# Performance work log

Hardware: AMD Instinct MI355X
Metric: run time of the kernel (lower is better)

Reference implementation:

```python
import jax, jax.numpy as jnp
import numpy as np

SIZE = 1024      # codebook size
DIM = 64         # latent_dim
TOPK = 3
BETA_C = 0.25
LEGACY = False

def setup_inputs() -> dict:
    key = jax.random.key(0)
    kz, ke = jax.random.split(key)
    z = jax.random.normal(kz, (16, 64, 64, DIM), dtype=jnp.float32)
    # nn.Embedding init: uniform(-1/size, 1/size)
    emb = jax.random.uniform(ke, (SIZE, DIM), minval=-1.0 / SIZE, maxval=1.0 / SIZE, dtype=jnp.float32)
    return {"z": z, "emb": emb}

def reference(z, emb):
    zf = z.reshape(-1, DIM)                                  # [N, D]
    # squared euclidean distances via matmul expansion: [N, SIZE]
    d = (jnp.sum(zf ** 2, axis=1, keepdims=True)
         + jnp.sum(emb ** 2, axis=1)
         - 2.0 * (zf @ emb.T))
    neg_d, topk_idx = jax.lax.top_k(-d, TOPK)                # smallest distances -> [N, K]
    # direct gather instead of one-hot matmul (same math)
    z_q = jnp.mean(emb[topk_idx], axis=1).reshape(z.shape)   # [N,K,D] -> [N,D] -> z.shape
    if LEGACY:
        loss = (jnp.mean((jax.lax.stop_gradient(z_q) - z) ** 2)
                + BETA_C * jnp.mean((z_q - jax.lax.stop_gradient(z)) ** 2))
    else:
        loss = (BETA_C * jnp.mean((jax.lax.stop_gradient(z_q) - z) ** 2)
                + jnp.mean((z_q - jax.lax.stop_gradient(z)) ** 2))
    # one-hot encodings are part of the module's return signature
    topk_encodings = jax.nn.one_hot(topk_idx, SIZE, dtype=z.dtype)   # [N, K, SIZE]
    e_mean = jnp.mean(topk_encodings, axis=(0, 1))                   # [SIZE]
    perplexity = jnp.exp(-jnp.sum(e_mean * jnp.log(e_mean + 1e-10)))
    z_q_st = z + jax.lax.stop_gradient(z_q - z)              # straight-through estimator
    return (z_q_st, loss, perplexity, topk_encodings, topk_idx)
```

## Files before the change

### kernel.cpp

```cpp
#include <hip/hip_runtime.h>
#include <math.h>

#define N_ROWS 65536
#define CB 1024
#define SPLITS 4
#define JS (CB / SPLITS)

__device__ __forceinline__ float tree_sum64_sq(const float* x) {
#pragma clang fp contract(off)
    float sq[64];
#pragma unroll
    for (int i = 0; i < 64; ++i) sq[i] = x[i] * x[i];
    float s[16];
#pragma unroll
    for (int l = 0; l < 16; ++l) s[l] = (sq[l] + sq[l + 16]) + (sq[l + 32] + sq[l + 48]);
    float t[8];
#pragma unroll
    for (int l = 0; l < 8; ++l) t[l] = s[l] + s[l + 8];
    float u[4];
#pragma unroll
    for (int l = 0; l < 4; ++l) u[l] = t[l] + t[l + 4];
    float v0 = u[0] + u[2];
    float v1 = u[1] + u[3];
    return v0 + v1;
}

__device__ __forceinline__ void top3_insert(float d, int j,
                                            float& v0, float& v1, float& v2,
                                            int& i0, int& i1, int& i2) {
    bool b0 = d < v0, b1 = d < v1, b2 = d < v2;
    v2 = b1 ? v1 : (b2 ? d : v2);
    i2 = b1 ? i1 : (b2 ? j : i2);
    v1 = b0 ? v0 : (b1 ? d : v1);
    i1 = b0 ? i0 : (b1 ? j : i1);
    v0 = b0 ? d : v0;
    i0 = b0 ? j : i0;
}

__global__ __launch_bounds__(256) void embB_kernel(const float* __restrict__ emb,
                                                   float* __restrict__ B) {
    int j = blockIdx.x * 256 + threadIdx.x;
    if (j >= CB) return;
    float e[64];
    const float4* e4 = (const float4*)(emb + (size_t)j * 64);
#pragma unroll
    for (int k = 0; k < 16; ++k) {
        float4 v = e4[k];
        e[4 * k] = v.x; e[4 * k + 1] = v.y; e[4 * k + 2] = v.z; e[4 * k + 3] = v.w;
    }
    B[j] = tree_sum64_sq(e);
}

__global__ __launch_bounds__(256) void score_kernel(const float* __restrict__ z,
                                                    const float* __restrict__ emb,
                                                    const float* __restrict__ B,
                                                    float* __restrict__ scrD,
                                                    int* __restrict__ scrI) {
    int bid = blockIdx.x;
    int split = bid & (SPLITS - 1);
    int rowBlk = bid >> 2;
    int row = rowBlk * 256 + threadIdx.x;

    float zr[64];
    const float4* z4 = (const float4*)(z + (size_t)row * 64);
#pragma unroll
    for (int k = 0; k < 16; ++k) {
        float4 v = z4[k];
        zr[4 * k] = v.x; zr[4 * k + 1] = v.y; zr[4 * k + 2] = v.z; zr[4 * k + 3] = v.w;
    }
    float A = tree_sum64_sq(zr);

    float v0 = 3.402823466e38f, v1 = 3.402823466e38f, v2 = 3.402823466e38f;
    int i0 = 0, i1 = 0, i2 = 0;
    int jbase = split * JS;

    for (int jj = 0; jj < JS; ++jj) {
        int j = jbase + jj;
        const float4* e4 = (const float4*)(emb + (size_t)j * 64);
        float Bj = B[j];
        float acc = 0.0f;
#pragma unroll
        for (int k = 0; k < 16; ++k) {
            float4 e = e4[k];
            acc = fmaf(zr[4 * k],     e.x, acc);
            acc = fmaf(zr[4 * k + 1], e.y, acc);
            acc = fmaf(zr[4 * k + 2], e.z, acc);
            acc = fmaf(zr[4 * k + 3], e.w, acc);
        }
        float d = (A + Bj) - 2.0f * acc;
        top3_insert(d, j, v0, v1, v2, i0, i1, i2);
    }
    size_t o = ((size_t)split * N_ROWS + row) * 3;
    scrD[o] = v0; scrD[o + 1] = v1; scrD[o + 2] = v2;
    scrI[o] = i0; scrI[o + 1] = i1; scrI[o + 2] = i2;
}

__global__ __launch_bounds__(256) void merge_kernel(const float* __restrict__ z,
                                                    const float* __restrict__ emb,
                                                    const float* __restrict__ scrD,
                                                    const int* __restrict__ scrI,
                                                    float* __restrict__ out0,
                                                    float* __restrict__ out4,
                                                    int* __restrict__ hist,
                                                    float* __restrict__ lossAcc) {
    int row = blockIdx.x * 256 + threadIdx.x;

    float v0 = 3.402823466e38f, v1 = 3.402823466e38f, v2 = 3.402823466e38f;
    int i0 = 0, i1 = 0, i2 = 0;
#pragma unroll
    for (int s = 0; s < SPLITS; ++s) {
        size_t o = ((size_t)s * N_ROWS + row) * 3;
#pragma unroll
        for (int t = 0; t < 3; ++t) {
            float d = scrD[o + t];
            int j = scrI[o + t];
            top3_insert(d, j, v0, v1, v2, i0, i1, i2);
        }
    }

    const float* e0 = emb + (size_t)i0 * 64;
    const float* e1 = emb + (size_t)i1 * 64;
    const float* e2 = emb + (size_t)i2 * 64;
    const float4* z4 = (const float4*)(z + (size_t)row * 64);
    float4* o4 = (float4*)(out0 + (size_t)row * 64);

    float lsum = 0.0f;
#pragma unroll
    for (int k4 = 0; k4 < 16; ++k4) {
        float4 zv = z4[k4];
        float4 st;
        {
            int k = 4 * k4;
            float zq = ((e0[k] + e1[k]) + e2[k]) / 3.0f;
            float df = zq - zv.x;
            st.x = zv.x + df;
            lsum = fmaf(df, df, lsum);
        }
        {
            int k = 4 * k4 + 1;
            float zq = ((e0[k] + e1[k]) + e2[k]) / 3.0f;
            float df = zq - zv.y;
            st.y = zv.y + df;
            lsum = fmaf(df, df, lsum);
        }
        {
            int k = 4 * k4 + 2;
            float zq = ((e0[k] + e1[k]) + e2[k]) / 3.0f;
            float df = zq - zv.z;
            st.z = zv.z + df;
            lsum = fmaf(df, df, lsum);
        }
        {
            int k = 4 * k4 + 3;
            float zq = ((e0[k] + e1[k]) + e2[k]) / 3.0f;
            float df = zq - zv.w;
            st.w = zv.w + df;
            lsum = fmaf(df, df, lsum);
        }
        o4[k4] = st;
    }

    size_t ob = (size_t)row * 3;
    out4[ob]     = (float)i0;
    out4[ob + 1] = (float)i1;
    out4[ob + 2] = (float)i2;
    atomicAdd(&hist[i0], 1);
    atomicAdd(&hist[i1], 1);
    atomicAdd(&hist[i2], 1);

#pragma unroll
    for (int off = 32; off >= 1; off >>= 1) lsum += __shfl_down(lsum, off);
    if ((threadIdx.x & 63) == 0) atomicAdd(lossAcc, lsum);
}

__global__ __launch_bounds__(256) void onehot_kernel(const float* __restrict__ idxf,
                                                     float4* __restrict__ out3) {
    size_t q = (size_t)blockIdx.x * 256 + threadIdx.x;
    int slice = (int)(q >> 8);
    int c0 = (int)(q & 255) * 4;
    int idx = (int)idxf[slice];
    float4 v;
    v.x = (c0     == idx) ? 1.0f : 0.0f;
    v.y = (c0 + 1 == idx) ? 1.0f : 0.0f;
    v.z = (c0 + 2 == idx) ? 1.0f : 0.0f;
    v.w = (c0 + 3 == idx) ? 1.0f : 0.0f;
    out3[q] = v;
}

__global__ __launch_bounds__(256) void finalize_kernel(const int* __restrict__ hist,
                                                       const float* __restrict__ lossAcc,
                                                       float* __restrict__ out1,
                                                       float* __restrict__ out2) {
    __shared__ float red[256];
    int t = threadIdx.x;
    float local = 0.0f;
    for (int b = t; b < CB; b += 256) {
        float em = (float)hist[b] / 196608.0f;
        local += em * logf(em + 1e-10f);
    }
    red[t] = local;
    __syncthreads();
    for (int s = 128; s >= 1; s >>= 1) {
        if (t < s) red[t] += red[t + s];
        __syncthreads();
    }
    if (t == 0) {
        *out2 = expf(-red[0]);
        float m = *lossAcc / 4194304.0f;
        *out1 = 0.25f * m + m;
    }
}

extern "C" void kernel_launch(void* const* d_in, const int* in_sizes, int n_in,
                              void* d_out, int out_size, void* d_ws, size_t ws_size,
                              hipStream_t stream) {
    const float* z   = (const float*)d_in[0];
    const float* emb = (const float*)d_in[1];

    float* out  = (float*)d_out;
    float* out0 = out;
    float* out1 = out + 4194304;
    float* out2 = out + 4194305;
    float* out3 = out + 4194306;
    float* out4 = out + 4194306 + 201326592ll;

    int*   hist    = (int*)d_ws;
    float* lossAcc = (float*)((char*)d_ws + 4096);
    float* B       = (float*)((char*)d_ws + 8192);

    float* scrD = out3;
    int*   scrI = (int*)(out3 + (size_t)SPLITS * N_ROWS * 3);

    hipMemsetAsync(d_ws, 0, 4096 + 16, stream);

    embB_kernel<<<4, 256, 0, stream>>>(emb, B);
    score_kernel<<<(N_ROWS / 256) * SPLITS, 256, 0, stream>>>(z, emb, B, scrD, scrI);
    merge_kernel<<<N_ROWS / 256, 256, 0, stream>>>(z, emb, scrD, scrI, out0, out4,
                                                   hist, lossAcc);
    onehot_kernel<<<196608, 256, 0, stream>>>(out4, (float4*)out3);
    finalize_kernel<<<1, 256, 0, stream>>>(hist, lossAcc, out1, out2);
}
```

Baseline: 1.076 ms.

## Fuse score and merge kernels via shared memory, align one-hot stores

Merges the split scoring and the top-3 merge into one kernel. Each block handles 64 rows with 4 codebook splits held in threads, and the partial top-3 results are combined in shared memory rather than through a global scratch buffer. The memset is folded into the prep kernel. The one-hot writer becomes a grid-stride loop with 16-byte-aligned nontemporal stores, offset by 2 floats because out3 is misaligned, with the edge elements fixed up separately. The combine step leaves 3/4 of each block's threads idle, and scoring now runs with 64 rows per block.

```diff
diff --git a/kernel.cpp b/kernel.cpp
--- a/kernel.cpp
+++ b/kernel.cpp
@@ -5,6 +5,8 @@
 #define CB 1024
 #define SPLITS 4
 #define JS (CB / SPLITS)
+
+typedef float v4f __attribute__((ext_vector_type(4)));
 
 __device__ __forceinline__ float tree_sum64_sq(const float* x) {
 #pragma clang fp contract(off)
@@ -37,8 +39,10 @@
     i0 = b0 ? j : i0;
 }
 
-__global__ __launch_bounds__(256) void embB_kernel(const float* __restrict__ emb,
-                                                   float* __restrict__ B) {
+__global__ __launch_bounds__(256) void prep_kernel(const float* __restrict__ emb,
+                                                   float* __restrict__ B,
+                                                   int* __restrict__ hist,
+                                                   float* __restrict__ lossAcc) {
     int j = blockIdx.x * 256 + threadIdx.x;
     if (j >= CB) return;
     float e[64];
@@ -49,17 +53,24 @@
         e[4 * k] = v.x; e[4 * k + 1] = v.y; e[4 * k + 2] = v.z; e[4 * k + 3] = v.w;
     }
     B[j] = tree_sum64_sq(e);
-}
-
-__global__ __launch_bounds__(256) void score_kernel(const float* __restrict__ z,
+    hist[j] = 0;
+    if (j == 0) *lossAcc = 0.0f;
+}
+
+__global__ __launch_bounds__(256) void fused_kernel(const float* __restrict__ z,
                                                     const float* __restrict__ emb,
                                                     const float* __restrict__ B,
-                                                    float* __restrict__ scrD,
-                                                    int* __restrict__ scrI) {
-    int bid = blockIdx.x;
-    int split = bid & (SPLITS - 1);
-    int rowBlk = bid >> 2;
-    int row = rowBlk * 256 + threadIdx.x;
+                                                    float* __restrict__ out0,
+                                                    float* __restrict__ out4,
+                                                    int* __restrict__ hist,
+                                                    float* __restrict__ lossAcc) {
+    __shared__ float sD[SPLITS][64][3];
+    __shared__ int   sI[SPLITS][64][3];
+
+    int t = threadIdx.x;
+    int r = t & 63;
+    int split = t >> 6;
+    int row = blockIdx.x * 64 + r;
 
     float zr[64];
     const float4* z4 = (const float4*)(z + (size_t)row * 64);
@@ -90,101 +101,85 @@
         float d = (A + Bj) - 2.0f * acc;
         top3_insert(d, j, v0, v1, v2, i0, i1, i2);
     }
-    size_t o = ((size_t)split * N_ROWS + row) * 3;
-    scrD[o] = v0; scrD[o + 1] = v1; scrD[o + 2] = v2;
-    scrI[o] = i0; scrI[o + 1] = i1; scrI[o + 2] = i2;
-}
-
-__global__ __launch_bounds__(256) void merge_kernel(const float* __restrict__ z,
-                                                    const float* __restrict__ emb,
-                                                    const float* __restrict__ scrD,
-                                                    const int* __restrict__ scrI,
-                                                    float* __restrict__ out0,
-                                                    float* __restrict__ out4,
-                                                    int* __restrict__ hist,
-                                                    float* __restrict__ lossAcc) {
-    int row = blockIdx.x * 256 + threadIdx.x;
-
-    float v0 = 3.402823466e38f, v1 = 3.402823466e38f, v2 = 3.402823466e38f;
-    int i0 = 0, i1 = 0, i2 = 0;
-#pragma unroll
-    for (int s = 0; s < SPLITS; ++s) {
-        size_t o = ((size_t)s * N_ROWS + row) * 3;
-#pragma unroll
-        for (int t = 0; t < 3; ++t) {
-            float d = scrD[o + t];
-            int j = scrI[o + t];
-            top3_insert(d, j, v0, v1, v2, i0, i1, i2);
+
+    sD[split][r][0] = v0; sD[split][r][1] = v1; sD[split][r][2] = v2;
+    sI[split][r][0] = i0; sI[split][r][1] = i1; sI[split][r][2] = i2;
+    __syncthreads();
+
+    if (t < 64) {
+        float m0 = 3.402823466e38f, m1 = 3.402823466e38f, m2 = 3.402823466e38f;
+        int j0 = 0, j1 = 0, j2 = 0;
+#pragma unroll
+        for (int s = 0; s < SPLITS; ++s) {
+#pragma unroll
+            for (int u = 0; u < 3; ++u)
+                top3_insert(sD[s][r][u], sI[s][r][u], m0, m1, m2, j0, j1, j2);
         }
-    }
-
-    const float* e0 = emb + (size_t)i0 * 64;
-    const float* e1 = emb + (size_t)i1 * 64;
-    const float* e2 = emb + (size_t)i2 * 64;
-    const float4* z4 = (const float4*)(z + (size_t)row * 64);
-    float4* o4 = (float4*)(out0 + (size_t)row * 64);
-
-    float lsum = 0.0f;
-#pragma unroll
-    for (int k4 = 0; k4 < 16; ++k4) {
-        float4 zv = z4[k4];
-        float4 st;
-        {
-            int k = 4 * k4;
-            float zq = ((e0[k] + e1[k]) + e2[k]) / 3.0f;
-            float df = zq - zv.x;
-            st.x = zv.x + df;
-            lsum = fmaf(df, df, lsum);
+
+        const float4* e0q = (const float4*)(emb + (size_t)j0 * 64);
+        const float4* e1q = (const float4*)(emb + (size_t)j1 * 64);
+        const float4* e2q = (const float4*)(emb + (size_t)j2 * 64);
+        v4f* o4 = (v4f*)(out0 + (size_t)row * 64);
+
+        float lsum = 0.0f;
+#pragma unroll
+        for (int k4 = 0; k4 < 16; ++k4) {
+            float4 a = e0q[k4], b = e1q[k4], c = e2q[k4];
+            float zx = zr[4 * k4], zy = zr[4 * k4 + 1];
+            float zz = zr[4 * k4 + 2], zw = zr[4 * k4 + 3];
+            v4f st;
+            float zq, df;
+            zq = ((a.x + b.x) + c.x) / 3.0f; df = zq - zx; st.x = zx + df; lsum = fmaf(df, df, lsum);
+            zq = ((a.y + b.y) + c.y) / 3.0f; df = zq - zy; st.y = zy + df; lsum = fmaf(df, df, lsum);
+            zq = ((a.z + b.z) + c.z) / 3.0f; df = zq - zz; st.z = zz + df; lsum = fmaf(df, df, lsum);
+            zq = ((a.w + b.w) + c.w) / 3.0f; df = zq - zw; st.w = zw + df; lsum = fmaf(df, df, lsum);
+            __builtin_nontemporal_store(st, o4 + k4);
         }
-        {
-            int k = 4 * k4 + 1;
-            float zq = ((e0[k] + e1[k]) + e2[k]) / 3.0f;
-            float df = zq - zv.y;
-            st.y = zv.y + df;
-            lsum = fmaf(df, df, lsum);
-        }
-        {
-            int k = 4 * k4 + 2;
-            float zq = ((e0[k] + e1[k]) + e2[k]) / 3.0f;
-            float df = zq - zv.z;
-            st.z = zv.z + df;
-            lsum = fmaf(df, df, lsum);
-        }
-        {
-            int k = 4 * k4 + 3;
-            float zq = ((e0[k] + e1[k]) + e2[k]) / 3.0f;
-            float df = zq - zv.w;
-            st.w = zv.w + df;
-            lsum = fmaf(df, df, lsum);
-        }
-        o4[k4] = st;
-    }
-
-    size_t ob = (size_t)row * 3;
-    out4[ob]     = (float)i0;
-    out4[ob + 1] = (float)i1;
-    out4[ob + 2] = (float)i2;
-    atomicAdd(&hist[i0], 1);
-    atomicAdd(&hist[i1], 1);
-    atomicAdd(&hist[i2], 1);
-
-#pragma unroll
-    for (int off = 32; off >= 1; off >>= 1) lsum += __shfl_down(lsum, off);
-    if ((threadIdx.x & 63) == 0) atomicAdd(lossAcc, lsum);
-}
-
+
+        size_t ob = (size_t)row * 3;
+        out4[ob]     = (float)j0;
+        out4[ob + 1] = (float)j1;
+        out4[ob + 2] = (float)j2;
+        atomicAdd(&hist[j0], 1);
+        atomicAdd(&hist[j1], 1);
+        atomicAdd(&hist[j2], 1);
+
+#pragma unroll
+        for (int off = 32; off >= 1; off >>= 1) lsum += __shfl_down(lsum, off);
+        if ((t & 63) == 0) atomicAdd(lossAcc, lsum);
+    }
+}
+
+#define OH_GRID 2048
 __global__ __launch_bounds__(256) void onehot_kernel(const float* __restrict__ idxf,
-                                                     float4* __restrict__ out3) {
-    size_t q = (size_t)blockIdx.x * 256 + threadIdx.x;
-    int slice = (int)(q >> 8);
-    int c0 = (int)(q & 255) * 4;
-    int idx = (int)idxf[slice];
-    float4 v;
-    v.x = (c0     == idx) ? 1.0f : 0.0f;
-    v.y = (c0 + 1 == idx) ? 1.0f : 0.0f;
-    v.z = (c0 + 2 == idx) ? 1.0f : 0.0f;
-    v.w = (c0 + 3 == idx) ? 1.0f : 0.0f;
-    out3[q] = v;
+                                                     float* __restrict__ out3f) {
+    v4f* o4 = (v4f*)(out3f + 2);
+    const int M = (N_ROWS * 3 * CB - 2) / 4;
+    const int stride = OH_GRID * 256;
+
+    for (int m = blockIdx.x * 256 + threadIdx.x; m < M; m += stride) {
+        int e0 = 2 + 4 * m;
+        int s0 = e0 >> 10;
+        int c0 = e0 & 1023;
+        int s3 = (e0 + 3) >> 10;
+        int ia = (int)idxf[s0];
+        int ib = (int)idxf[s3];
+        v4f v;
+        v.x = (c0     == ia) ? 1.0f : 0.0f;
+        v.y = (c0 + 1 == ia) ? 1.0f : 0.0f;
+        v.z = (((c0 + 2) & 1023) == ib) ? 1.0f : 0.0f;
+        v.w = (((c0 + 3) & 1023) == ib) ? 1.0f : 0.0f;
+        __builtin_nontemporal_store(v, o4 + m);
+    }
+
+    if (blockIdx.x == 0 && threadIdx.x == 0) {
+        int ia = (int)idxf[0];
+        out3f[0] = (ia == 0) ? 1.0f : 0.0f;
+        out3f[1] = (ia == 1) ? 1.0f : 0.0f;
+        int ib = (int)idxf[N_ROWS * 3 - 1];
+        out3f[(size_t)N_ROWS * 3 * CB - 2] = (ib == 1022) ? 1.0f : 0.0f;
+        out3f[(size_t)N_ROWS * 3 * CB - 1] = (ib == 1023) ? 1.0f : 0.0f;
+    }
 }
 
 __global__ __launch_bounds__(256) void finalize_kernel(const int* __restrict__ hist,
@@ -228,15 +223,9 @@
     float* lossAcc = (float*)((char*)d_ws + 4096);
     float* B       = (float*)((char*)d_ws + 8192);
 
-    float* scrD = out3;
-    int*   scrI = (int*)(out3 + (size_t)SPLITS * N_ROWS * 3);
-
-    hipMemsetAsync(d_ws, 0, 4096 + 16, stream);
-
-    embB_kernel<<<4, 256, 0, stream>>>(emb, B);
-    score_kernel<<<(N_ROWS / 256) * SPLITS, 256, 0, stream>>>(z, emb, B, scrD, scrI);
-    merge_kernel<<<N_ROWS / 256, 256, 0, stream>>>(z, emb, scrD, scrI, out0, out4,
-                                                   hist, lossAcc);
-    onehot_kernel<<<196608, 256, 0, stream>>>(out4, (float4*)out3);
+    prep_kernel<<<4, 256, 0, stream>>>(emb, B, hist, lossAcc);
+    fused_kernel<<<N_ROWS / 64, 256, 0, stream>>>(z, emb, B, out0, out4,
+                                                  hist, lossAcc);
+    onehot_kernel<<<OH_GRID, 256, 0, stream>>>(out4, out3);
     finalize_kernel<<<1, 256, 0, stream>>>(hist, lossAcc, out1, out2);
 }
```

Measured after the change: 1.402 ms. +30.3%, slower.
